# Optimization experiments

Measured on AMD Instinct MI355X. Metric: run time of the kernel, lower is better.

The kernel has to match this reference:

```python
import jax, jax.numpy as jnp
import numpy as np

NUM_SENTENCES = 32
MAX_SENT_LEN = 64
EMBED_DIM = 768
BATCH = 16
TEXT_LEN = NUM_SENTENCES * MAX_SENT_LEN  # 2048


def setup_inputs() -> dict:
    key = jax.random.key(0)
    k1, k2 = jax.random.split(key)
    inputs = jax.random.normal(k1, (BATCH, TEXT_LEN, EMBED_DIM), dtype=jnp.float32)
    W = jax.random.normal(k2, (EMBED_DIM, 2 * NUM_SENTENCES), dtype=jnp.float32) * 0.02
    b = jnp.zeros((2 * NUM_SENTENCES,), dtype=jnp.float32)
    return {"inputs": inputs, "W": W, "b": b}


def reference(inputs, W, b):
    B, T, E = inputs.shape
    S, L = NUM_SENTENCES, MAX_SENT_LEN

    # offsets from mean-pooled input through Dense(2*S)
    pooled = jnp.mean(inputs, axis=1)                      # [B, E]
    offsets = pooled @ W + b                               # [B, 2S]
    # clip to [0, L-1], cast (truncation == floor for nonneg values)
    start_off = jnp.clip(offsets[:, :S], 0.0, float(L - 1)).astype(jnp.int32)  # [B, S]
    end_off = jnp.clip(offsets[:, S:], 0.0, float(L - 1)).astype(jnp.int32)    # [B, S]

    base = (jnp.arange(S, dtype=jnp.int32) * L)[None, :]   # [1, S]
    start_idx = jnp.clip(base + start_off, 0, T - L)        # [B, S]
    end_idx = jnp.clip(base + L + end_off, start_idx, T)    # [B, S]

    # vectorized slice+pad: position j of sentence i comes from start_idx+j,
    # valid while j < (end_idx - start_idx) and j < L (pad/truncate to L)
    j = jnp.arange(L, dtype=jnp.int32)                      # [L]
    gather_idx = start_idx[:, :, None] + j[None, None, :]   # [B, S, L]
    valid = j[None, None, :] < (end_idx - start_idx)[:, :, None]  # [B, S, L]

    flat_idx = jnp.clip(gather_idx, 0, T - 1).reshape(B, S * L)
    gathered = jnp.take_along_axis(inputs, flat_idx[:, :, None], axis=1)
    gathered = gathered.reshape(B, S, L, E)
    out = jnp.where(valid[:, :, :, None], gathered, jnp.zeros((), inputs.dtype))
    return out
```

## Files before the change

kernel.cpp:

```cpp
#include <hip/hip_runtime.h>

#define BATCH 16
#define T_LEN 2048
#define E_DIM 768
#define E4 (E_DIM / 4)
#define N_SENT 32
#define S_LEN 64
#define NCHUNK 64
#define ROWS_PER_CHUNK (T_LEN / NCHUNK)

typedef float nf4 __attribute__((ext_vector_type(4)));

__global__ void pool_partial(const float4* __restrict__ in4, float4* __restrict__ partial4) {
    const int tx = threadIdx.x;
    const int b  = blockIdx.x;
    const int tc = blockIdx.y;
    const float4* p = in4 + ((size_t)b * T_LEN + (size_t)tc * ROWS_PER_CHUNK) * E4 + tx;
    float4 s = make_float4(0.f, 0.f, 0.f, 0.f);
#pragma unroll 8
    for (int t = 0; t < ROWS_PER_CHUNK; ++t) {
        float4 v = p[(size_t)t * E4];
        s.x += v.x; s.y += v.y; s.z += v.z; s.w += v.w;
    }
    partial4[((size_t)tc * BATCH + b) * E4 + tx] = s;
}

__global__ void compute_idx(const float4* __restrict__ partial4,
                            const float* __restrict__ W,
                            const float* __restrict__ bias,
                            int* __restrict__ sidx, int* __restrict__ eidx) {
    __shared__ float pooled[E_DIM];
    __shared__ float colsum[4][2 * N_SENT];
    __shared__ int   offi[2 * N_SENT];
    const int b   = blockIdx.x;
    const int tid = threadIdx.x;

    if (tid < E4) {
        float4 s = make_float4(0.f, 0.f, 0.f, 0.f);
#pragma unroll 8
        for (int tc = 0; tc < NCHUNK; ++tc) {
            float4 v = partial4[((size_t)tc * BATCH + b) * E4 + tid];
            s.x += v.x; s.y += v.y; s.z += v.z; s.w += v.w;
        }
        const float inv = 1.0f / (float)T_LEN;
        ((float4*)pooled)[tid] = make_float4(s.x * inv, s.y * inv, s.z * inv, s.w * inv);
    }
    __syncthreads();

    const int c = tid & 63;
    const int q = tid >> 6;
    float acc = 0.f;
    const float* pb = pooled + q * 192;
    const float* Wq = W + (size_t)q * 192 * (2 * N_SENT) + c;
#pragma unroll 8
    for (int e = 0; e < 192; ++e) acc += pb[e] * Wq[(size_t)e * (2 * N_SENT)];
    colsum[q][c] = acc;
    __syncthreads();

    if (tid < 2 * N_SENT) {
        float o = bias[tid] + colsum[0][tid] + colsum[1][tid] + colsum[2][tid] + colsum[3][tid];
        float cl = fminf(fmaxf(o, 0.f), (float)(S_LEN - 1));
        offi[tid] = (int)cl;
    }
    __syncthreads();

    if (tid < N_SENT) {
        const int so   = offi[tid];
        const int eo   = offi[N_SENT + tid];
        const int base = tid * S_LEN;
        int si = min(base + so, T_LEN - S_LEN);
        int ei = min(max(base + S_LEN + eo, si), T_LEN);
        sidx[b * N_SENT + tid] = si;
        eidx[b * N_SENT + tid] = ei;
    }
}

__global__ __launch_bounds__(256) void gather_rows(const float4* __restrict__ in4,
                                                   const int* __restrict__ sidx,
                                                   const int* __restrict__ eidx,
                                                   float4* __restrict__ out4) {
    const int blk  = blockIdx.x;
    const int half = blk & 1;
    const int s    = (blk >> 1) & (N_SENT - 1);
    const int b    = blk >> 6;
    const int lane = threadIdx.x & 63;
    const int q    = threadIdx.x >> 6;

    const int si  = sidx[b * N_SENT + s];
    const int ei  = eidx[b * N_SENT + s];
    const int len = ei - si;

    const float4* src = in4  + ((size_t)b * T_LEN + si) * E4 + lane;
    float4*       dst = out4 + (((size_t)b * N_SENT + s) * S_LEN) * E4 + lane;
    const float4 z = make_float4(0.f, 0.f, 0.f, 0.f);

#pragma unroll 4
    for (int k = 0; k < 8; ++k) {
        const int j = half * 32 + q * 8 + k;
        float4 v0 = z, v1 = z, v2 = z;
        if (j < len) {
            const float4* sp = src + (size_t)j * E4;
            v0 = sp[0]; v1 = sp[64]; v2 = sp[128];
        }
        nf4* dp = (nf4*)(dst + (size_t)j * E4);
        __builtin_nontemporal_store(*(const nf4*)&v0, dp);
        __builtin_nontemporal_store(*(const nf4*)&v1, dp + 64);
        __builtin_nontemporal_store(*(const nf4*)&v2, dp + 128);
    }
}

extern "C" void kernel_launch(void* const* d_in, const int* in_sizes, int n_in,
                              void* d_out, int out_size, void* d_ws, size_t ws_size,
                              hipStream_t stream) {
    const float4* in4 = (const float4*)d_in[0];
    const float*  W   = (const float*)d_in[1];
    const float*  bias= (const float*)d_in[2];
    float4* out4 = (float4*)d_out;

    float4* partial4 = (float4*)d_ws;
    int* sidx = (int*)((char*)d_ws + (size_t)NCHUNK * BATCH * E4 * sizeof(float4));
    int* eidx = sidx + BATCH * N_SENT;

    pool_partial<<<dim3(BATCH, NCHUNK), 192, 0, stream>>>(in4, partial4);
    compute_idx<<<BATCH, 256, 0, stream>>>(partial4, W, bias, sidx, eidx);
    gather_rows<<<dim3(BATCH * N_SENT * 2), 256, 0, stream>>>(in4, sidx, eidx, out4);
}
```

Before: 208.0 us.

## Fuse index computation into gather kernel and halve pooling chunks

Removes the separate compute_idx kernel by having each gather block re-reduce the pooled partials and compute its own sentence's start/end offsets. Two threads per block each do a 768-length dot product for their column. NCHUNK drops from 64 to 32, so the pooling kernel launches fewer, longer blocks and each gather block has fewer partials to reduce. This saves one launch and a global round-trip for the indices. In exchange, the partial reduction is repeated redundantly in all 1024 blocks, and a serial dot product on two threads now sits before every block's copy.

```diff
diff --git a/kernel.cpp b/kernel.cpp
--- a/kernel.cpp
+++ b/kernel.cpp
@@ -6,7 +6,7 @@
 #define E4 (E_DIM / 4)
 #define N_SENT 32
 #define S_LEN 64
-#define NCHUNK 64
+#define NCHUNK 32
 #define ROWS_PER_CHUNK (T_LEN / NCHUNK)
 
 typedef float nf4 __attribute__((ext_vector_type(4)));
@@ -25,70 +25,60 @@
     partial4[((size_t)tc * BATCH + b) * E4 + tx] = s;
 }
 
-__global__ void compute_idx(const float4* __restrict__ partial4,
-                            const float* __restrict__ W,
-                            const float* __restrict__ bias,
-                            int* __restrict__ sidx, int* __restrict__ eidx) {
-    __shared__ float pooled[E_DIM];
-    __shared__ float colsum[4][2 * N_SENT];
-    __shared__ int   offi[2 * N_SENT];
-    const int b   = blockIdx.x;
-    const int tid = threadIdx.x;
-
-    if (tid < E4) {
-        float4 s = make_float4(0.f, 0.f, 0.f, 0.f);
-#pragma unroll 8
-        for (int tc = 0; tc < NCHUNK; ++tc) {
-            float4 v = partial4[((size_t)tc * BATCH + b) * E4 + tid];
-            s.x += v.x; s.y += v.y; s.z += v.z; s.w += v.w;
-        }
-        const float inv = 1.0f / (float)T_LEN;
-        ((float4*)pooled)[tid] = make_float4(s.x * inv, s.y * inv, s.z * inv, s.w * inv);
-    }
-    __syncthreads();
-
-    const int c = tid & 63;
-    const int q = tid >> 6;
-    float acc = 0.f;
-    const float* pb = pooled + q * 192;
-    const float* Wq = W + (size_t)q * 192 * (2 * N_SENT) + c;
-#pragma unroll 8
-    for (int e = 0; e < 192; ++e) acc += pb[e] * Wq[(size_t)e * (2 * N_SENT)];
-    colsum[q][c] = acc;
-    __syncthreads();
-
-    if (tid < 2 * N_SENT) {
-        float o = bias[tid] + colsum[0][tid] + colsum[1][tid] + colsum[2][tid] + colsum[3][tid];
-        float cl = fminf(fmaxf(o, 0.f), (float)(S_LEN - 1));
-        offi[tid] = (int)cl;
-    }
-    __syncthreads();
-
-    if (tid < N_SENT) {
-        const int so   = offi[tid];
-        const int eo   = offi[N_SENT + tid];
-        const int base = tid * S_LEN;
-        int si = min(base + so, T_LEN - S_LEN);
-        int ei = min(max(base + S_LEN + eo, si), T_LEN);
-        sidx[b * N_SENT + tid] = si;
-        eidx[b * N_SENT + tid] = ei;
-    }
-}
-
-__global__ __launch_bounds__(256) void gather_rows(const float4* __restrict__ in4,
-                                                   const int* __restrict__ sidx,
-                                                   const int* __restrict__ eidx,
-                                                   float4* __restrict__ out4) {
+__global__ __launch_bounds__(256) void gather_idx_rows(
+    const float4* __restrict__ in4,
+    const float4* __restrict__ partial4,
+    const float*  __restrict__ W,
+    const float*  __restrict__ bias,
+    float4* __restrict__ out4)
+{
     const int blk  = blockIdx.x;
     const int half = blk & 1;
     const int s    = (blk >> 1) & (N_SENT - 1);
     const int b    = blk >> 6;
-    const int lane = threadIdx.x & 63;
-    const int q    = threadIdx.x >> 6;
+    const int tid  = threadIdx.x;
+    const int lane = tid & 63;
+    const int q    = tid >> 6;
 
-    const int si  = sidx[b * N_SENT + s];
-    const int ei  = eidx[b * N_SENT + s];
-    const int len = ei - si;
+    __shared__ float pooled[E_DIM];
+    __shared__ int   sie[2];
+
+    if (tid < E4) {
+        float4 acc = make_float4(0.f, 0.f, 0.f, 0.f);
+#pragma unroll 8
+        for (int tc = 0; tc < NCHUNK; ++tc) {
+            float4 v = partial4[((size_t)tc * BATCH + b) * E4 + tid];
+            acc.x += v.x; acc.y += v.y; acc.z += v.z; acc.w += v.w;
+        }
+        const float inv = 1.0f / (float)T_LEN;
+        ((float4*)pooled)[tid] = make_float4(acc.x * inv, acc.y * inv, acc.z * inv, acc.w * inv);
+    }
+    __syncthreads();
+
+    if (tid < 2) {
+        const int c = s + tid * N_SENT;
+        float qacc[4];
+#pragma unroll
+        for (int qq = 0; qq < 4; ++qq) {
+            float acc = 0.f;
+            const float* pb = pooled + qq * 192;
+            const float* Wq = W + (size_t)qq * 192 * (2 * N_SENT) + c;
+#pragma unroll 8
+            for (int e = 0; e < 192; ++e) acc += pb[e] * Wq[(size_t)e * (2 * N_SENT)];
+            qacc[qq] = acc;
+        }
+        float o  = bias[c] + qacc[0] + qacc[1] + qacc[2] + qacc[3];
+        float cl = fminf(fmaxf(o, 0.f), (float)(S_LEN - 1));
+        sie[tid] = (int)cl;
+    }
+    __syncthreads();
+
+    const int so   = sie[0];
+    const int eo   = sie[1];
+    const int base = s * S_LEN;
+    const int si   = min(base + so, T_LEN - S_LEN);
+    const int ei   = min(max(base + S_LEN + eo, si), T_LEN);
+    const int len  = ei - si;
 
     const float4* src = in4  + ((size_t)b * T_LEN + si) * E4 + lane;
     float4*       dst = out4 + (((size_t)b * N_SENT + s) * S_LEN) * E4 + lane;
@@ -118,10 +108,8 @@
     float4* out4 = (float4*)d_out;
 
     float4* partial4 = (float4*)d_ws;
-    int* sidx = (int*)((char*)d_ws + (size_t)NCHUNK * BATCH * E4 * sizeof(float4));
-    int* eidx = sidx + BATCH * N_SENT;
 
     pool_partial<<<dim3(BATCH, NCHUNK), 192, 0, stream>>>(in4, partial4);
-    compute_idx<<<BATCH, 256, 0, stream>>>(partial4, W, bias, sidx, eidx);
-    gather_rows<<<dim3(BATCH * N_SENT * 2), 256, 0, stream>>>(in4, sidx, eidx, out4);
+    gather_idx_rows<<<dim3(BATCH * N_SENT * 2), 256, 0, stream>>>(
+        in4, partial4, W, bias, out4);
 }
```

New measurement: 237.8 us. +14.3%, slower.
